# Optimization experiments

Hardware: AMD Instinct MI355X
Metric: run time of the kernel (lower is better)

## Reference

```python
import jax, jax.numpy as jnp
import numpy as np


def setup_inputs() -> dict:
    key = jax.random.key(0)
    ks = jax.random.split(key, 5)
    T, B, E = 2048, 2, 1024
    return {
        "query": jax.random.normal(ks[0], (T, B, E), dtype=jnp.float32),
        "in_proj_weight": jax.random.normal(ks[1], (3 * E, E), dtype=jnp.float32) * (E ** -0.5),
        "in_proj_bias": jax.random.normal(ks[2], (3 * E,), dtype=jnp.float32) * 0.02,
        "out_proj_weight": jax.random.normal(ks[3], (E, E), dtype=jnp.float32) * (E ** -0.5),
        "out_proj_bias": jax.random.normal(ks[4], (E,), dtype=jnp.float32) * 0.02,
        "num_heads": 16,
    }


def reference(query, in_proj_weight, in_proj_bias, out_proj_weight, out_proj_bias, num_heads):
    T, B, E = query.shape
    H = num_heads
    d = E // H
    scaling = d ** -0.5
    # fused QKV projection: (T,B,E) @ (E,3E) + bias -> (T,B,3E)
    qkv = jnp.einsum('tbe,fe->tbf', query, in_proj_weight) + in_proj_bias
    # torch views (T*B, 3E) as (T, B*H, 3, d): per token layout is (H, 3, d)
    qkv = qkv.reshape(T, B, H, 3, d)
    q = qkv[..., 0, :] * scaling  # (T,B,H,d)
    k = qkv[..., 1, :]
    v = qkv[..., 2, :]
    scores = jnp.einsum('tbhd,sbhd->bhts', q, k)  # (B,H,T,T)
    probs = jax.nn.softmax(scores.astype(jnp.float32), axis=-1).astype(scores.dtype)
    ctx = jnp.einsum('bhts,sbhd->tbhd', probs, v).reshape(T, B, E)
    out = jnp.einsum('tbe,fe->tbf', ctx, out_proj_weight) + out_proj_bias
    return out
```

## Files before the change

### kernel.cpp

```cpp
#include <hip/hip_runtime.h>
#include <hip/hip_bf16.h>
#include <math.h>

constexpr int T_DIM = 2048;
constexpr int B_DIM = 2;
constexpr int E_DIM = 1024;
constexpr float QK_SCALE = 0.18033688011112042f;

#if __has_builtin(__builtin_amdgcn_exp2f)
#define EXP2F(x) __builtin_amdgcn_exp2f(x)
#else
#define EXP2F(x) exp2f(x)
#endif

typedef __attribute__((ext_vector_type(8))) short short8;
typedef __attribute__((ext_vector_type(4))) float f32x4;

__device__ inline short f2bf(float x) {
    union { __hip_bfloat16 b; short s; } u;
    u.b = __float2bfloat16(x);
    return u.s;
}
__device__ inline float bf2f(short s) {
    union { __hip_bfloat16 b; short s; } u;
    u.s = s;
    return __bfloat162float(u.b);
}

__device__ inline int pack_bf16(float hi, float lo) {
    union { float f; unsigned u; } a, b;
    a.f = hi; b.f = lo;
    return (int)__builtin_amdgcn_perm(a.u + 0x8000u, b.u + 0x8000u, 0x07060302u);
}

__device__ inline void gl2lds16(const void* g, void* l) {
    __builtin_amdgcn_global_load_lds(
        (const __attribute__((address_space(1))) unsigned int*)g,
        (__attribute__((address_space(3))) unsigned int*)l, 16, 0, 0);
}

__device__ inline f32x4 mfma_bf16(short8 a, short8 b, f32x4 c) {
    return __builtin_amdgcn_mfma_f32_16x16x32_bf16(a, b, c, 0, 0, 0);
}

__global__ __launch_bounds__(256)
void split_all_kernel(const float* __restrict__ query,
                      const float* __restrict__ w_in,
                      const float* __restrict__ w_out,
                      short* __restrict__ qh,
                      short* __restrict__ wih, short* __restrict__ wil,
                      short* __restrict__ woh, short* __restrict__ wol,
                      int nq4, int nwi4, int nwo4)
{
    int i = blockIdx.x * 256 + threadIdx.x;
    const float* src; short* dh; short* dl; int k; int do_lo;
    if (i < nq4) { src = query; dh = qh; dl = nullptr; k = i; do_lo = 0; }
    else if (i < nq4 + nwi4) { src = w_in; dh = wih; dl = wil; k = i - nq4; do_lo = 1; }
    else { src = w_out; dh = woh; dl = wol; k = i - nq4 - nwi4; do_lo = 1; }
    float4 v = ((const float4*)src)[k];
    short h0 = f2bf(v.x), h1 = f2bf(v.y), h2 = f2bf(v.z), h3 = f2bf(v.w);
    ((short4*)dh)[k] = make_short4(h0, h1, h2, h3);
    if (do_lo) {
        short l0 = f2bf(v.x - bf2f(h0));
        short l1 = f2bf(v.y - bf2f(h1));
        short l2 = f2bf(v.z - bf2f(h2));
        short l3 = f2bf(v.w - bf2f(h3));
        ((short4*)dl)[k] = make_short4(l0, l1, l2, l3);
    }
}

__global__ __launch_bounds__(256)
void gemm_in(const short* __restrict__ Ah,
             const short* __restrict__ Wh, const short* __restrict__ Wl,
             const float* __restrict__ bias,
             short* __restrict__ qkv, short* __restrict__ kp,
             short* __restrict__ vtp,
             int M, int N, int K)
{
    __shared__ __align__(16) short AsH[128 * 32];
    __shared__ __align__(16) short WsH[128 * 32];
    __shared__ __align__(16) short WsL[128 * 32];

    const int tid  = threadIdx.x;
    const int lane = tid & 63;
    const int wave = tid >> 6;
    const int rm = (wave >> 1) * 64;
    const int cn = (wave & 1) * 64;
    const int m0 = blockIdx.y * 128;
    const int n0 = blockIdx.x * 128;

    const int srow0 = wave * 32 + (lane >> 2);
    const int srow1 = srow0 + 16;
    const int p4 = lane & 3;
    const int kc0 = p4 ^ ((srow0 >> 1) & 3);
    const int kc1 = p4 ^ ((srow1 >> 1) & 3);

    short* ldsA0 = &AsH[(wave * 32) * 32];
    short* ldsA1 = &AsH[(wave * 32 + 16) * 32];
    short* ldsW0 = &WsH[(wave * 32) * 32];
    short* ldsW1 = &WsH[(wave * 32 + 16) * 32];
    short* ldsWl0 = &WsL[(wave * 32) * 32];
    short* ldsWl1 = &WsL[(wave * 32 + 16) * 32];

    const size_t ga0 = (size_t)(m0 + srow0) * K + kc0 * 8;
    const size_t ga1 = (size_t)(m0 + srow1) * K + kc1 * 8;
    const size_t gw0 = (size_t)(n0 + srow0) * K + kc0 * 8;
    const size_t gw1 = (size_t)(n0 + srow1) * K + kc1 * 8;

    const f32x4 zero = {0.f, 0.f, 0.f, 0.f};
    f32x4 acc[4][4];
    #pragma unroll
    for (int i = 0; i < 4; ++i)
        #pragma unroll
        for (int j = 0; j < 4; ++j) acc[i][j] = zero;

    const int fr = lane & 15;
    const int qc = lane >> 4;

    for (int k0 = 0; k0 < K; k0 += 32) {
        if (k0) __syncthreads();
        gl2lds16(Ah + ga0 + k0, ldsA0);
        gl2lds16(Ah + ga1 + k0, ldsA1);
        gl2lds16(Wh + gw0 + k0, ldsW0);
        gl2lds16(Wh + gw1 + k0, ldsW1);
        gl2lds16(Wl + gw0 + k0, ldsWl0);
        gl2lds16(Wl + gw1 + k0, ldsWl1);
        __syncthreads();

        short8 ahf[4], bhf[4], blf[4];
        #pragma unroll
        for (int i = 0; i < 4; ++i) {
            int r = rm + 16 * i + fr;
            int slot = qc ^ ((r >> 1) & 3);
            ahf[i] = *(const short8*)&AsH[r * 32 + slot * 8];
        }
        #pragma unroll
        for (int j = 0; j < 4; ++j) {
            int r = cn + 16 * j + fr;
            int slot = qc ^ ((r >> 1) & 3);
            bhf[j] = *(const short8*)&WsH[r * 32 + slot * 8];
            blf[j] = *(const short8*)&WsL[r * 32 + slot * 8];
        }
        #pragma unroll
        for (int i = 0; i < 4; ++i)
            #pragma unroll
            for (int j = 0; j < 4; ++j) {
                acc[i][j] = mfma_bf16(ahf[i], bhf[j], acc[i][j]);
                acc[i][j] = mfma_bf16(ahf[i], blf[j], acc[i][j]);
            }
    }

    const int g = lane >> 4;
    #pragma unroll
    for (int j = 0; j < 4; ++j) {
        const int colu = n0 + cn + 16 * j;
        const int col  = colu + fr;
        const float bj = bias[col];
        const int c6  = colu >> 6;
        const int grp = c6 % 3;
        const int h   = c6 / 3;
        const int d   = (colu & 63) + fr;
        if (grp == 0) {
            #pragma unroll
            for (int i = 0; i < 4; ++i)
                #pragma unroll
                for (int r = 0; r < 4; ++r) {
                    int row = m0 + rm + 16 * i + g * 4 + r;
                    qkv[(size_t)row * 3072 + col] =
                        f2bf((acc[i][j][r] + bj) * QK_SCALE);
                }
        } else if (grp == 1) {
            const int hh = d >> 5, gk = (d >> 3) & 3, ii = d & 7;
            #pragma unroll
            for (int i = 0; i < 4; ++i)
                #pragma unroll
                for (int r = 0; r < 4; ++r) {
                    int row = m0 + rm + 16 * i + g * 4 + r;
                    int t = row >> 1, bb = row & 1;
                    int m = t & 63;
                    int R = (m & 32) | ((m & 24) >> 1) | ((m & 4) << 2) | (m & 3);
                    size_t off = (size_t)(bb * 16 + h) * 131072
                               + (size_t)(t >> 6) * 4096
                               + (size_t)(((2 * (R >> 4) + hh) * 64
                                           + gk * 16 + (R & 15)) * 8 + ii);
                    kp[off] = f2bf(acc[i][j][r] + bj);
                }
        } else {
            const int jd = d >> 4, frv = d & 15;
            #pragma unroll
            for (int i = 0; i < 4; ++i)
                #pragma unroll
                for (int r = 0; r < 4; ++r) {
                    int row = m0 + rm + 16 * i + g * 4 + r;
                    int t = row >> 1, bb = row & 1;
                    int tl = t & 63;
                    size_t off = (size_t)(bb * 16 + h) * 131072
                               + (size_t)(t >> 6) * 4096
                               + (size_t)(((2 * jd + (tl >> 5)) * 64
                                           + ((tl >> 3) & 3) * 16 + frv) * 8
                                          + (tl & 7));
                    vtp[off] = f2bf(acc[i][j][r] + bj);
                }
        }
    }
}

__global__ __launch_bounds__(256)
void gemm_out(const short* __restrict__ Ah, const short* __restrict__ Al,
              const short* __restrict__ Wh, const short* __restrict__ Wl,
              const float* __restrict__ bias, float* __restrict__ Cout,
              int M, int N, int K)
{
    __shared__ __align__(16) short AsH[64 * 32];
    __shared__ __align__(16) short AsL[64 * 32];
    __shared__ __align__(16) short WsH[128 * 32];
    __shared__ __align__(16) short WsL[128 * 32];

    const int tid  = threadIdx.x;
    const int lane = tid & 63;
    const int wave = tid >> 6;
    const int m0 = blockIdx.y * 64;
    const int n0 = blockIdx.x * 128;

    const int arow = wave * 16 + (lane >> 2);
    const int akc = (lane & 3) ^ ((arow >> 1) & 3);
    const size_t gaA = (size_t)(m0 + arow) * K + akc * 8;
    const int wrow0 = wave * 32 + (lane >> 2);
    const int wrow1 = wrow0 + 16;
    const int wkc0 = (lane & 3) ^ ((wrow0 >> 1) & 3);
    const int wkc1 = (lane & 3) ^ ((wrow1 >> 1) & 3);
    const size_t gw0 = (size_t)(n0 + wrow0) * K + wkc0 * 8;
    const size_t gw1 = (size_t)(n0 + wrow1) * K + wkc1 * 8;

    short* ldsAh = &AsH[wave * 512];
    short* ldsAl = &AsL[wave * 512];
    short* ldsW0 = &WsH[(wave * 2) * 512];
    short* ldsW1 = &WsH[(wave * 2 + 1) * 512];
    short* ldsWl0 = &WsL[(wave * 2) * 512];
    short* ldsWl1 = &WsL[(wave * 2 + 1) * 512];

    const f32x4 zero = {0.f, 0.f, 0.f, 0.f};
    f32x4 acc[4][2];
    #pragma unroll
    for (int i = 0; i < 4; ++i) { acc[i][0] = zero; acc[i][1] = zero; }

    const int fr = lane & 15;
    const int g = lane >> 4;

    for (int k0 = 0; k0 < K; k0 += 32) {
        if (k0) __syncthreads();
        gl2lds16(Ah + gaA + k0, ldsAh);
        gl2lds16(Al + gaA + k0, ldsAl);
        gl2lds16(Wh + gw0 + k0, ldsW0);
        gl2lds16(Wh + gw1 + k0, ldsW1);
        gl2lds16(Wl + gw0 + k0, ldsWl0);
        gl2lds16(Wl + gw1 + k0, ldsWl1);
        __syncthreads();

        short8 ahf[4], alf[4], bhf[2], blf[2];
        #pragma unroll
        for (int i = 0; i < 4; ++i) {
            int r = 16 * i + fr;
            int slot = g ^ ((r >> 1) & 3);
            ahf[i] = *(const short8*)&AsH[r * 32 + slot * 8];
            alf[i] = *(const short8*)&AsL[r * 32 + slot * 8];
        }
        #pragma unroll
        for (int j = 0; j < 2; ++j) {
            int r = wave * 32 + 16 * j + fr;
            int slot = g ^ ((r >> 1) & 3);
            bhf[j] = *(const short8*)&WsH[r * 32 + slot * 8];
            blf[j] = *(const short8*)&WsL[r * 32 + slot * 8];
        }
        #pragma unroll
        for (int i = 0; i < 4; ++i)
            #pragma unroll
            for (int j = 0; j < 2; ++j) {
                acc[i][j] = mfma_bf16(ahf[i], bhf[j], acc[i][j]);
                acc[i][j] = mfma_bf16(ahf[i], blf[j], acc[i][j]);
                acc[i][j] = mfma_bf16(alf[i], bhf[j], acc[i][j]);
            }
    }

    #pragma unroll
    for (int j = 0; j < 2; ++j) {
        int col = n0 + wave * 32 + 16 * j + fr;
        float bj = bias[col];
        #pragma unroll
        for (int i = 0; i < 4; ++i)
            #pragma unroll
            for (int r = 0; r < 4; ++r) {
                int row = m0 + 16 * i + g * 4 + r;
                Cout[(size_t)row * N + col] = acc[i][j][r] + bj;
            }
    }
}

__global__ __launch_bounds__(256, 2)
void attn_mfma(const short* __restrict__ qkv, const short* __restrict__ kp,
               const short* __restrict__ vtp,
               short* __restrict__ ctxh, short* __restrict__ ctxl)
{
    __shared__ __align__(16) short ldsK[2][4096];
    __shared__ __align__(16) short ldsV[2][4096];

    const int tid  = threadIdx.x;
    const int lane = tid & 63;
    const int wave = tid >> 6;
    const int fr = lane & 15;
    const int g  = lane >> 4;

    const int id = blockIdx.x;
    const int x = id & 7, y = id >> 3;
    const int bh = x * 4 + (y & 3);
    const int q0 = (y >> 2) * 128;
    const int b = bh >> 4, h = bh & 15;

    short8 aq[2][2];
    #pragma unroll
    for (int set = 0; set < 2; ++set) {
        const short* qrow = qkv +
            ((size_t)(q0 + wave * 32 + set * 16 + fr) * 2 + b) * 3072 + h * 192;
        aq[set][0] = *(const short8*)(qrow + g * 8);
        aq[set][1] = *(const short8*)(qrow + 32 + g * 8);
    }

    const short* kt = kp  + (size_t)bh * 131072;
    const short* vt = vtp + (size_t)bh * 131072;

    short8 ONES;
    #pragma unroll
    for (int i = 0; i < 8; ++i) ONES[i] = (short)0x3F80;

    const f32x4 zero = {0.f, 0.f, 0.f, 0.f};
    f32x4 o[2][4];
    #pragma unroll
    for (int set = 0; set < 2; ++set)
        #pragma unroll
        for (int jd = 0; jd < 4; ++jd) o[set][jd] = zero;
    f32x4 lacc[2] = {zero, zero};

    auto stage = [&](int it, int sel) {
        const short* ks = kt + it * 4096 + wave * 1024 + lane * 8;
        const short* vs = vt + it * 4096 + wave * 1024 + lane * 8;
        gl2lds16(ks,       &ldsK[sel][wave * 1024]);
        gl2lds16(ks + 512, &ldsK[sel][wave * 1024 + 512]);
        gl2lds16(vs,       &ldsV[sel][wave * 1024]);
        gl2lds16(vs + 512, &ldsV[sel][wave * 1024 + 512]);
    };

    stage(0, 0);
    #pragma unroll 2
    for (int it = 0; it < 32; ++it) {
        const int cur = it & 1;
        __syncthreads();
        if (it + 1 < 32) stage(it + 1, cur ^ 1);

        int afw[2][2][4];
        #pragma unroll
        for (int s = 0; s < 4; ++s) {
            short8 k0 = *(const short8*)&ldsK[cur][(2 * s) * 512 + lane * 8];
            short8 k1 = *(const short8*)&ldsK[cur][(2 * s + 1) * 512 + lane * 8];
            #pragma unroll
            for (int set = 0; set < 2; ++set) {
                f32x4 a = zero;
                a = mfma_bf16(k0, aq[set][0], a);
                a = mfma_bf16(k1, aq[set][1], a);
                float e0 = EXP2F(a[0]), e1 = EXP2F(a[1]);
                float e2 = EXP2F(a[2]), e3 = EXP2F(a[3]);
                afw[set][s >> 1][(s & 1) * 2]     = pack_bf16(e1, e0);
                afw[set][s >> 1][(s & 1) * 2 + 1] = pack_bf16(e3, e2);
            }
        }
        union { int w[4]; short8 v; } A[2][2];
        #pragma unroll
        for (int set = 0; set < 2; ++set)
            #pragma unroll
            for (int hh = 0; hh < 2; ++hh)
                #pragma unroll
                for (int w = 0; w < 4; ++w) A[set][hh].w[w] = afw[set][hh][w];

        #pragma unroll
        for (int set = 0; set < 2; ++set) {
            lacc[set] = mfma_bf16(A[set][0].v, ONES, lacc[set]);
            lacc[set] = mfma_bf16(A[set][1].v, ONES, lacc[set]);
        }

        #pragma unroll
        for (int jd = 0; jd < 4; ++jd) {
            short8 v0 = *(const short8*)&ldsV[cur][(2 * jd) * 512 + lane * 8];
            short8 v1 = *(const short8*)&ldsV[cur][(2 * jd + 1) * 512 + lane * 8];
            #pragma unroll
            for (int set = 0; set < 2; ++set) {
                o[set][jd] = mfma_bf16(A[set][0].v, v0, o[set][jd]);
                o[set][jd] = mfma_bf16(A[set][1].v, v1, o[set][jd]);
            }
        }
    }

    #pragma unroll
    for (int set = 0; set < 2; ++set)
        #pragma unroll
        for (int r = 0; r < 4; ++r) {
            float inv = 1.f / lacc[set][r];
            int t = q0 + wave * 32 + set * 16 + 4 * g + r;
            size_t base = ((size_t)t * B_DIM + b) * E_DIM + h * 64;
            #pragma unroll
            for (int jd = 0; jd < 4; ++jd) {
                float v = o[set][jd][r] * inv;
                short hs = f2bf(v);
                short ls = f2bf(v - bf2f(hs));
                ctxh[base + 16 * jd + fr] = hs;
                ctxl[base + 16 * jd + fr] = ls;
            }
        }
}

extern "C" void kernel_launch(void* const* d_in, const int* in_sizes, int n_in,
                              void* d_out, int out_size, void* d_ws, size_t ws_size,
                              hipStream_t stream)
{
    const float* query = (const float*)d_in[0];
    const float* w_in  = (const float*)d_in[1];
    const float* b_in  = (const float*)d_in[2];
    const float* w_out = (const float*)d_in[3];
    const float* b_out = (const float*)d_in[4];
    float* out = (float*)d_out;

    char* ws = (char*)d_ws;
    short* qkv  = (short*)(ws);
    short* qh   = (short*)(ws + 25165824);
    short* wih  = (short*)(ws + 33554432);
    short* wil  = (short*)(ws + 39845888);
    short* woh  = (short*)(ws + 46137344);
    short* wol  = (short*)(ws + 48234496);
    short* vtp  = (short*)(ws + 50331648);
    short* kp   = (short*)(ws + 58720256);
    short* ctxh = (short*)(ws + 25165824);
    short* ctxl = (short*)(ws + 33554432);

    const int M = T_DIM * B_DIM;

    int nq4  = (M * E_DIM) / 4;
    int nwi4 = (3 * E_DIM * E_DIM) / 4;
    int nwo4 = (E_DIM * E_DIM) / 4;
    split_all_kernel<<<(nq4 + nwi4 + nwo4) / 256, 256, 0, stream>>>(
        query, w_in, w_out, qh, wih, wil, woh, wol, nq4, nwi4, nwo4);

    gemm_in<<<dim3(3 * E_DIM / 128, M / 128), 256, 0, stream>>>(
        qh, wih, wil, b_in, qkv, kp, vtp, M, 3 * E_DIM, E_DIM);

    attn_mfma<<<dim3(512), 256, 0, stream>>>(qkv, kp, vtp, ctxh, ctxl);

    gemm_out<<<dim3(E_DIM / 128, M / 64), 256, 0, stream>>>(
        ctxh, ctxl, woh, wol, b_out, out, M, E_DIM, E_DIM);
}
```

Before: 215.8 us.

## Use 128x128 tiles with split-K and a separate reduce for output projection

The output-projection GEMM moves from 64x128 block tiles to 128x128 tiles, with each wave computing a 64x64 sub-tile. K is split in two across blockIdx.z so the grid stays at 512 blocks. Each half writes fp32 partial sums into workspace regions that are dead after attention, and a new reduce kernel adds the two partials plus the bias. This improves operand reuse per MFMA, at the cost of an extra kernel launch and roughly 48MB of extra global traffic for writing and re-reading the partials.

```diff
diff --git a/kernel.cpp b/kernel.cpp
--- a/kernel.cpp
+++ b/kernel.cpp
@@ -206,93 +206,122 @@
 }
 
 __global__ __launch_bounds__(256)
-void gemm_out(const short* __restrict__ Ah, const short* __restrict__ Al,
-              const short* __restrict__ Wh, const short* __restrict__ Wl,
-              const float* __restrict__ bias, float* __restrict__ Cout,
-              int M, int N, int K)
-{
-    __shared__ __align__(16) short AsH[64 * 32];
-    __shared__ __align__(16) short AsL[64 * 32];
+void gemm_out_ks(const short* __restrict__ Ah, const short* __restrict__ Al,
+                 const short* __restrict__ Wh, const short* __restrict__ Wl,
+                 float* __restrict__ part0, float* __restrict__ part1,
+                 int M, int N, int K)
+{
+    __shared__ __align__(16) short AsH[128 * 32];
+    __shared__ __align__(16) short AsL[128 * 32];
     __shared__ __align__(16) short WsH[128 * 32];
     __shared__ __align__(16) short WsL[128 * 32];
 
     const int tid  = threadIdx.x;
     const int lane = tid & 63;
     const int wave = tid >> 6;
-    const int m0 = blockIdx.y * 64;
+    const int rm = (wave >> 1) * 64;
+    const int cn = (wave & 1) * 64;
+    const int m0 = blockIdx.y * 128;
     const int n0 = blockIdx.x * 128;
-
-    const int arow = wave * 16 + (lane >> 2);
-    const int akc = (lane & 3) ^ ((arow >> 1) & 3);
-    const size_t gaA = (size_t)(m0 + arow) * K + akc * 8;
-    const int wrow0 = wave * 32 + (lane >> 2);
-    const int wrow1 = wrow0 + 16;
-    const int wkc0 = (lane & 3) ^ ((wrow0 >> 1) & 3);
-    const int wkc1 = (lane & 3) ^ ((wrow1 >> 1) & 3);
-    const size_t gw0 = (size_t)(n0 + wrow0) * K + wkc0 * 8;
-    const size_t gw1 = (size_t)(n0 + wrow1) * K + wkc1 * 8;
-
-    short* ldsAh = &AsH[wave * 512];
-    short* ldsAl = &AsL[wave * 512];
-    short* ldsW0 = &WsH[(wave * 2) * 512];
-    short* ldsW1 = &WsH[(wave * 2 + 1) * 512];
-    short* ldsWl0 = &WsL[(wave * 2) * 512];
-    short* ldsWl1 = &WsL[(wave * 2 + 1) * 512];
+    const int kbeg = blockIdx.z * 512;
+    float* __restrict__ part = blockIdx.z ? part1 : part0;
+
+    const int srow0 = wave * 32 + (lane >> 2);
+    const int srow1 = srow0 + 16;
+    const int p4 = lane & 3;
+    const int kc0 = p4 ^ ((srow0 >> 1) & 3);
+    const int kc1 = p4 ^ ((srow1 >> 1) & 3);
+
+    short* ldsAh0 = &AsH[(wave * 32) * 32];
+    short* ldsAh1 = &AsH[(wave * 32 + 16) * 32];
+    short* ldsAl0 = &AsL[(wave * 32) * 32];
+    short* ldsAl1 = &AsL[(wave * 32 + 16) * 32];
+    short* ldsWh0 = &WsH[(wave * 32) * 32];
+    short* ldsWh1 = &WsH[(wave * 32 + 16) * 32];
+    short* ldsWl0 = &WsL[(wave * 32) * 32];
+    short* ldsWl1 = &WsL[(wave * 32 + 16) * 32];
+
+    const size_t ga0 = (size_t)(m0 + srow0) * K + kbeg + kc0 * 8;
+    const size_t ga1 = (size_t)(m0 + srow1) * K + kbeg + kc1 * 8;
+    const size_t gw0 = (size_t)(n0 + srow0) * K + kbeg + kc0 * 8;
+    const size_t gw1 = (size_t)(n0 + srow1) * K + kbeg + kc1 * 8;
 
     const f32x4 zero = {0.f, 0.f, 0.f, 0.f};
-    f32x4 acc[4][2];
-    #pragma unroll
-    for (int i = 0; i < 4; ++i) { acc[i][0] = zero; acc[i][1] = zero; }
+    f32x4 acc[4][4];
+    #pragma unroll
+    for (int i = 0; i < 4; ++i)
+        #pragma unroll
+        for (int j = 0; j < 4; ++j) acc[i][j] = zero;
 
     const int fr = lane & 15;
-    const int g = lane >> 4;
-
-    for (int k0 = 0; k0 < K; k0 += 32) {
+    const int qc = lane >> 4;
+
+    for (int k0 = 0; k0 < 512; k0 += 32) {
         if (k0) __syncthreads();
-        gl2lds16(Ah + gaA + k0, ldsAh);
-        gl2lds16(Al + gaA + k0, ldsAl);
-        gl2lds16(Wh + gw0 + k0, ldsW0);
-        gl2lds16(Wh + gw1 + k0, ldsW1);
+        gl2lds16(Ah + ga0 + k0, ldsAh0);
+        gl2lds16(Ah + ga1 + k0, ldsAh1);
+        gl2lds16(Al + ga0 + k0, ldsAl0);
+        gl2lds16(Al + ga1 + k0, ldsAl1);
+        gl2lds16(Wh + gw0 + k0, ldsWh0);
+        gl2lds16(Wh + gw1 + k0, ldsWh1);
         gl2lds16(Wl + gw0 + k0, ldsWl0);
         gl2lds16(Wl + gw1 + k0, ldsWl1);
         __syncthreads();
 
-        short8 ahf[4], alf[4], bhf[2], blf[2];
+        short8 ahf[4], alf[4], bhf[4], blf[4];
         #pragma unroll
         for (int i = 0; i < 4; ++i) {
-            int r = 16 * i + fr;
-            int slot = g ^ ((r >> 1) & 3);
+            int r = rm + 16 * i + fr;
+            int slot = qc ^ ((r >> 1) & 3);
             ahf[i] = *(const short8*)&AsH[r * 32 + slot * 8];
             alf[i] = *(const short8*)&AsL[r * 32 + slot * 8];
         }
         #pragma unroll
-        for (int j = 0; j < 2; ++j) {
-            int r = wave * 32 + 16 * j + fr;
-            int slot = g ^ ((r >> 1) & 3);
+        for (int j = 0; j < 4; ++j) {
+            int r = cn + 16 * j + fr;
+            int slot = qc ^ ((r >> 1) & 3);
             bhf[j] = *(const short8*)&WsH[r * 32 + slot * 8];
             blf[j] = *(const short8*)&WsL[r * 32 + slot * 8];
         }
         #pragma unroll
         for (int i = 0; i < 4; ++i)
             #pragma unroll
-            for (int j = 0; j < 2; ++j) {
+            for (int j = 0; j < 4; ++j) {
                 acc[i][j] = mfma_bf16(ahf[i], bhf[j], acc[i][j]);
                 acc[i][j] = mfma_bf16(ahf[i], blf[j], acc[i][j]);
                 acc[i][j] = mfma_bf16(alf[i], bhf[j], acc[i][j]);
             }
     }
 
-    #pragma unroll
-    for (int j = 0; j < 2; ++j) {
-        int col = n0 + wave * 32 + 16 * j + fr;
-        float bj = bias[col];
+    const int g = lane >> 4;
+    #pragma unroll
+    for (int j = 0; j < 4; ++j) {
+        int col = n0 + cn + 16 * j + fr;
         #pragma unroll
         for (int i = 0; i < 4; ++i)
             #pragma unroll
             for (int r = 0; r < 4; ++r) {
-                int row = m0 + 16 * i + g * 4 + r;
-                Cout[(size_t)row * N + col] = acc[i][j][r] + bj;
-            }
+                int row = m0 + rm + 16 * i + g * 4 + r;
+                part[(size_t)row * N + col] = acc[i][j][r];
+            }
+    }
+}
+
+__global__ __launch_bounds__(256)
+void reduce_out(const float* __restrict__ p0, const float* __restrict__ p1,
+                const float* __restrict__ bias, float* __restrict__ out,
+                int n4)
+{
+    for (int i = blockIdx.x * 256 + threadIdx.x; i < n4; i += gridDim.x * 256) {
+        float4 a = ((const float4*)p0)[i];
+        float4 b = ((const float4*)p1)[i];
+        float4 c = ((const float4*)bias)[i & 255];
+        float4 o;
+        o.x = a.x + b.x + c.x;
+        o.y = a.y + b.y + c.y;
+        o.z = a.z + b.z + c.z;
+        o.w = a.w + b.w + c.w;
+        ((float4*)out)[i] = o;
     }
 }
 
@@ -438,6 +467,8 @@
     short* kp   = (short*)(ws + 58720256);
     short* ctxh = (short*)(ws + 25165824);
     short* ctxl = (short*)(ws + 33554432);
+    float* p0   = (float*)(ws);
+    float* p1   = (float*)(ws + 50331648);
 
     const int M = T_DIM * B_DIM;
 
@@ -452,6 +483,8 @@
 
     attn_mfma<<<dim3(512), 256, 0, stream>>>(qkv, kp, vtp, ctxh, ctxl);
 
-    gemm_out<<<dim3(E_DIM / 128, M / 64), 256, 0, stream>>>(
-        ctxh, ctxl, woh, wol, b_out, out, M, E_DIM, E_DIM);
-}
+    gemm_out_ks<<<dim3(E_DIM / 128, M / 128, 2), 256, 0, stream>>>(
+        ctxh, ctxl, woh, wol, p0, p1, M, E_DIM, E_DIM);
+
+    reduce_out<<<2048, 256, 0, stream>>>(p0, p1, b_out, out, (M * E_DIM) / 4);
+}
```

New measurement: 227.3 us. 5.3% more time.
